# Kernel tuning notes

Measured on AMD Instinct MI355X. Metric: run time of the kernel, lower is better.

Reference implementation:

```python
import jax, jax.numpy as jnp
import numpy as np

N_NODES = 16384
N_EDGES = 65536
N_GRAPHS = 512
F_XD = 78
HEADS = 10
HID = F_XD * HEADS  # 780
SEQ = 1000
EMB = 100
VOCAB = 8000
NF = 32
KS = 8
CLEN = EMB - KS + 1  # 93
OUT_DIM = 128


def setup_inputs():
    key = jax.random.key(0)
    keys = jax.random.split(key, 32)
    it = iter(keys)

    def rn(shape, scale=0.05):
        return jax.random.normal(next(it), shape, dtype=jnp.float32) * scale

    x = jax.random.normal(next(it), (N_NODES, F_XD), dtype=jnp.float32)
    edge_index = jax.random.randint(next(it), (2, N_EDGES), 0, N_NODES)
    batch = jnp.sort(jax.random.randint(next(it), (N_NODES,), 0, N_GRAPHS))
    target = jax.random.randint(next(it), (N_GRAPHS, SEQ), 0, VOCAB)
    return {
        "x": x, "edge_index": edge_index, "batch": batch, "target": target,
        "gat_w": rn((F_XD, HID)), "gat_att_src": rn((HEADS, F_XD)),
        "gat_att_dst": rn((HEADS, F_XD)), "gat_b": rn((HID,)),
        "gcn_w": rn((HID, HID)), "gcn_b": rn((HID,)),
        "fcg1_w": rn((2 * HID, 1500)), "fcg1_b": rn((1500,)),
        "fcg2_w": rn((1500, OUT_DIM)), "fcg2_b": rn((OUT_DIM,)),
        "emb_w": rn((VOCAB, EMB), 1.0),
        "conv_w": rn((NF, SEQ, KS)), "conv_b": rn((NF,)),
        "fcxt_w": rn((NF * CLEN, OUT_DIM)), "fcxt_b": rn((OUT_DIM,)),
        "mlp1_w": rn((2 * OUT_DIM, 1024)), "mlp1_b": rn((1024,)),
        "mlp2_w": rn((1024, 512)), "mlp2_b": rn((512,)),
        "mlp3_w": rn((512, 1)), "mlp3_b": rn((1,)),
    }


def _forward(edge_index, batch, target, x, gat_w, gat_att_src, gat_att_dst, gat_b,
             gcn_w, gcn_b, fcg1_w, fcg1_b, fcg2_w, fcg2_b, emb_w, conv_w, conv_b,
             fcxt_w, fcxt_b, mlp1_w, mlp1_b, mlp2_w, mlp2_b, mlp3_w, mlp3_b):
    loops = jnp.arange(N_NODES)
    src = jnp.concatenate([edge_index[0], loops])  # add self-loops (PyG default)
    dst = jnp.concatenate([edge_index[1], loops])
    # --- GATConv(78 -> 78, heads=10, concat) ---
    xh = (x @ gat_w).reshape(N_NODES, HEADS, F_XD)
    a_src = jnp.einsum('nhc,hc->nh', xh, gat_att_src)
    a_dst = jnp.einsum('nhc,hc->nh', xh, gat_att_dst)
    e = jax.nn.leaky_relu(a_src[src] + a_dst[dst], 0.2)  # [E+N, H]
    emax = jax.ops.segment_max(e, dst, num_segments=N_NODES)
    ee = jnp.exp(e - emax[dst])
    den = jax.ops.segment_sum(ee, dst, num_segments=N_NODES)
    coef = ee / den[dst]  # segment softmax over incoming edges
    h = jax.ops.segment_sum(xh[src] * coef[:, :, None], dst, num_segments=N_NODES)
    h = jax.nn.relu(h.reshape(N_NODES, HID) + gat_b)
    # --- GCNConv(780 -> 780), symmetric normalization with self-loops ---
    hw = h @ gcn_w
    deg = jax.ops.segment_sum(jnp.ones((src.shape[0],), hw.dtype), dst, num_segments=N_NODES)
    dinv = jax.lax.rsqrt(jnp.maximum(deg, 1.0))  # deg >= 1 due to self-loops
    g = jax.ops.segment_sum(hw[src] * (dinv[src] * dinv[dst])[:, None], dst,
                            num_segments=N_NODES) + gcn_b
    g = jax.nn.relu(g)
    # --- global max / mean pool per graph ---
    gmp = jax.ops.segment_max(g, batch, num_segments=N_GRAPHS)
    cnt = jax.ops.segment_sum(jnp.ones((N_NODES,), g.dtype), batch, num_segments=N_GRAPHS)
    gap = jax.ops.segment_sum(g, batch, num_segments=N_GRAPHS) / jnp.maximum(cnt, 1.0)[:, None]
    d = jnp.concatenate([gmp, gap], axis=1)  # [B, 1560]
    d = jax.nn.relu(d @ fcg1_w + fcg1_b)     # dropout = eval-mode no-op
    d = d @ fcg2_w + fcg2_b                  # [B, 128]
    # --- protein branch: embedding + Conv1d(in=1000, out=32, k=8) + fc ---
    emb = emb_w[target]  # [B, SEQ=1000, EMB=100]
    c = jax.lax.conv_general_dilated(emb, conv_w, (1,), 'VALID',
                                     dimension_numbers=('NCH', 'OIH', 'NCH'))
    c = c + conv_b[None, :, None]            # [B, 32, 93]
    p = c.reshape(N_GRAPHS, NF * CLEN) @ fcxt_w + fcxt_b  # [B, 128]
    # --- fused MLP head: 256 -> 1024 -> 512 -> 1 ---
    o = jnp.concatenate([d, p], axis=1)
    o = jax.nn.relu(o @ mlp1_w + mlp1_b)
    o = jax.nn.relu(o @ mlp2_w + mlp2_b)
    return o @ mlp3_w + mlp3_b               # [B, 1]


def reference(x, edge_index, batch, target, gat_w, gat_att_src, gat_att_dst, gat_b,
              gcn_w, gcn_b, fcg1_w, fcg1_b, fcg2_w, fcg2_b, emb_w, conv_w, conv_b,
              fcxt_w, fcxt_b, mlp1_w, mlp1_b, mlp2_w, mlp2_b, mlp3_w, mlp3_b):
    return _forward(edge_index, batch, target, x, gat_w, gat_att_src, gat_att_dst,
                    gat_b, gcn_w, gcn_b, fcg1_w, fcg1_b, fcg2_w, fcg2_b, emb_w,
                    conv_w, conv_b, fcxt_w, fcxt_b, mlp1_w, mlp1_b, mlp2_w, mlp2_b,
                    mlp3_w, mlp3_b)
```

## Files before the change

### kernel.cpp

```cpp
#include <hip/hip_runtime.h>

#define NN 16384
#define NE 65536
#define NT 81920
#define NG 512
#define NH 10
#define FX 78
#define HD 780
#define SEQ 1000
#define EMB 100
#define NF 32
#define KS 8
#define CLEN 93

typedef __bf16 bf16x8 __attribute__((ext_vector_type(8)));
typedef float  f32x4  __attribute__((ext_vector_type(4)));

__device__ inline void load_lds16(const void* g, void* l)
{
    __builtin_amdgcn_global_load_lds(
        (const __attribute__((address_space(1))) void*)g,
        (__attribute__((address_space(3))) void*)l, 16, 0, 0);
}

__device__ inline void bt_one(const float* __restrict__ B, __bf16* __restrict__ out,
                              long idx, int K, int N, int Kp)
{
    int n = idx / Kp, k = idx - (long)(idx / Kp)*Kp;
    out[idx] = (n < N && k < K) ? (__bf16)B[(size_t)k*N + n] : (__bf16)0.f;
}

__global__ __launch_bounds__(256)
void preproc_all(const float* __restrict__ emb_w, __bf16* __restrict__ embbf,
                 const float* __restrict__ conv_w, __bf16* __restrict__ w2,
                 const float* __restrict__ fcg1_w, __bf16* __restrict__ wg1,
                 const float* __restrict__ fcg2_w, __bf16* __restrict__ wg2,
                 const float* __restrict__ fcxt_w, __bf16* __restrict__ wxt,
                 const float* __restrict__ mlp1_w, __bf16* __restrict__ wm1,
                 const float* __restrict__ mlp2_w, __bf16* __restrict__ wm2,
                 const float* __restrict__ x, __bf16* __restrict__ Abf,
                 const float* __restrict__ gat_w, __bf16* __restrict__ wgat,
                 const float* __restrict__ gcn_w, __bf16* __restrict__ wgcn,
                 const int* __restrict__ batch, int* __restrict__ goffs)
{
    long idx = (long)blockIdx.x*256 + threadIdx.x;
    if (idx < 896112L) {
        int r = idx / 112, c = idx - (long)(idx/112)*112;
        embbf[idx] = (__bf16)((r < 8000 && c < EMB) ? emb_w[(size_t)r*EMB + c] : 0.f);
        return;
    }
    idx -= 896112L;
    if (idx < 262144L) {
        int op = idx >> 10, i = idx & 1023;
        int o = op & 31, k = op >> 5;
        w2[idx] = (i < SEQ) ? (__bf16)conv_w[((size_t)o*SEQ + i)*KS + k] : (__bf16)0.f;
        return;
    }
    idx -= 262144L;
    if (idx < 2408448L) { bt_one(fcg1_w, wg1, idx, 1560, 1500, 1568); return; }
    idx -= 2408448L;
    if (idx < 192512L)  { bt_one(fcg2_w, wg2, idx, 1500, 128, 1504); return; }
    idx -= 192512L;
    if (idx < 380928L)  { bt_one(fcxt_w, wxt, idx, 2976, 128, 2976); return; }
    idx -= 380928L;
    if (idx < 262144L)  { bt_one(mlp1_w, wm1, idx, 256, 1024, 256); return; }
    idx -= 262144L;
    if (idx < 524288L)  { bt_one(mlp2_w, wm2, idx, 1024, 512, 1024); return; }
    idx -= 524288L;
    if (idx < 1572864L) {
        int r = idx / 96, c = idx - (long)(idx/96)*96;
        Abf[idx] = (c < FX) ? (__bf16)x[(size_t)r*FX + c] : (__bf16)0.f;
        return;
    }
    idx -= 1572864L;
    if (idx < 86016L)   { bt_one(gat_w, wgat, idx, 78, 780, 96); return; }
    idx -= 86016L;
    if (idx < 716800L)  { bt_one(gcn_w, wgcn, idx, 780, 780, 800); return; }
    idx -= 716800L;
    if (idx <= NG) {
        int b = (int)idx;
        if (b == NG) { goffs[NG] = NN; return; }
        int lo = 0, hi = NN;
        while (lo < hi) { int mid = (lo+hi) >> 1; if (batch[mid] < b) lo = mid+1; else hi = mid; }
        goffs[b] = lo;
    }
}
#define PRE_TOTAL 7302256L
#define PRE_BLOCKS ((PRE_TOTAL + 513 + 255) / 256)

template<bool BIAS, bool RELU, bool BF16OUT>
__global__ __launch_bounds__(512)
void gemm_mfma(const __bf16* __restrict__ A, const __bf16* __restrict__ Bt,
               const float* __restrict__ bias, void* __restrict__ Cv,
               int M, int N, int Kp, int ldc, int Nz)
{
    __shared__ __align__(16) __bf16 As[128*32];
    __shared__ __align__(16) __bf16 Bs[128*32];
    const int tid = threadIdx.x;
    const int nbx = gridDim.x;
    const int lin = blockIdx.y * nbx + blockIdx.x;
    const int per = (nbx * gridDim.y) >> 3;
    const int logical = (lin & 7) * per + (lin >> 3);
    const int row0 = (logical / nbx) * 128, col0 = (logical % nbx) * 128;
    const int lane = tid & 63, wid = tid >> 6;
    const int wm = wid & 3, wn = wid >> 2;
    const int l15 = lane & 15, lk = lane >> 4;
    const int sr  = tid >> 2;
    const int sc8 = (tid & 3) * 8;

    f32x4 acc[2][4];
#pragma unroll
    for (int i = 0; i < 2; i++)
#pragma unroll
        for (int j = 0; j < 4; j++) acc[i][j] = (f32x4){0.f,0.f,0.f,0.f};

    for (int k0 = 0; k0 < Kp; k0 += 32) {
        __syncthreads();
        load_lds16(A  + (size_t)(row0+sr)*Kp + k0 + sc8, &As[wid*512]);
        load_lds16(Bt + (size_t)(col0+sr)*Kp + k0 + sc8, &Bs[wid*512]);
        __syncthreads();
        bf16x8 af[2], bfr[4];
#pragma unroll
        for (int i = 0; i < 2; i++)
            af[i]  = *(const bf16x8*)&As[(wm*32 + i*16 + l15)*32 + lk*8];
#pragma unroll
        for (int j = 0; j < 4; j++)
            bfr[j] = *(const bf16x8*)&Bs[(wn*64 + j*16 + l15)*32 + lk*8];
#pragma unroll
        for (int i = 0; i < 2; i++)
#pragma unroll
            for (int j = 0; j < 4; j++)
                acc[i][j] = __builtin_amdgcn_mfma_f32_16x16x32_bf16(af[i], bfr[j], acc[i][j], 0, 0, 0);
    }

#pragma unroll
    for (int i = 0; i < 2; i++) {
        int rbase = row0 + wm*32 + i*16 + lk*4;
#pragma unroll
        for (int j = 0; j < 4; j++) {
            int cc = col0 + wn*64 + j*16 + l15;
            if (cc >= Nz) continue;
            bool real = cc < N;
            float bv = (BIAS && real) ? bias[cc] : 0.f;
#pragma unroll
            for (int r = 0; r < 4; r++) {
                float v = real ? (acc[i][j][r] + bv) : 0.f;
                if (RELU) v = v > 0.f ? v : 0.f;
                if (BF16OUT) ((__bf16*)Cv)[(size_t)(rbase + r)*ldc + cc] = (__bf16)v;
                else         ((float*) Cv)[(size_t)(rbase + r)*ldc + cc] = v;
            }
        }
    }
}

#define BKP 40
__global__ __launch_bounds__(256)
void gemm_mfma_splitk(const __bf16* __restrict__ A, const __bf16* __restrict__ Bt,
                      float* __restrict__ part, int M, int Kp, int ldp, int ksteps)
{
    __shared__ __align__(16) __bf16 As[128*BKP];
    __shared__ __align__(16) __bf16 Bs[128*BKP];
    const int tid = threadIdx.x;
    const int row0 = blockIdx.y*128, col0 = blockIdx.x*128;
    const int s = blockIdx.z;
    const int lane = tid & 63, wid = tid >> 6;
    const int wm = wid & 1, wn = wid >> 1;
    const int l15 = lane & 15, lk = lane >> 4;

    const int T = Kp >> 5;
    int kb = s*ksteps, ke = kb + ksteps;
    if (ke > T) ke = T;

    f32x4 acc[4][4];
#pragma unroll
    for (int i = 0; i < 4; i++)
#pragma unroll
        for (int j = 0; j < 4; j++) acc[i][j] = (f32x4){0.f,0.f,0.f,0.f};

    for (int kk = kb; kk < ke; kk++) {
        int k0 = kk*32;
        __syncthreads();
#pragma unroll
        for (int it = 0; it < 2; ++it) {
            int c = tid + it*256;
            int r = c >> 2, c16 = c & 3;
            uint4 va = *(const uint4*)(A  + (size_t)(row0+r)*Kp + k0 + c16*8);
            *(uint4*)&As[r*BKP + c16*8] = va;
            uint4 vb = *(const uint4*)(Bt + (size_t)(col0+r)*Kp + k0 + c16*8);
            *(uint4*)&Bs[r*BKP + c16*8] = vb;
        }
        __syncthreads();
        bf16x8 af[4], bfr[4];
#pragma unroll
        for (int i = 0; i < 4; i++) {
            af[i]  = *(const bf16x8*)&As[(wm*64 + i*16 + l15)*BKP + lk*8];
            bfr[i] = *(const bf16x8*)&Bs[(wn*64 + i*16 + l15)*BKP + lk*8];
        }
#pragma unroll
        for (int i = 0; i < 4; i++)
#pragma unroll
            for (int j = 0; j < 4; j++)
                acc[i][j] = __builtin_amdgcn_mfma_f32_16x16x32_bf16(af[i], bfr[j], acc[i][j], 0, 0, 0);
    }

#pragma unroll
    for (int i = 0; i < 4; i++) {
        int rbase = row0 + wm*64 + i*16 + lk*4;
#pragma unroll
        for (int j = 0; j < 4; j++) {
            int cc = col0 + wn*64 + j*16 + l15;
#pragma unroll
            for (int r = 0; r < 4; r++)
                part[((size_t)s*M + rbase + r)*ldp + cc] = acc[i][j][r];
        }
    }
}

template<bool RELU>
__global__ __launch_bounds__(256)
void reduce_splitk(const float* __restrict__ part, const float* __restrict__ bias,
                   __bf16* __restrict__ C, int M, int N, int ldp, int S,
                   int ldc, int Nz)
{
    int idx = blockIdx.x*256 + threadIdx.x;
    int nc4 = Nz >> 2;
    if (idx >= M*nc4) return;
    int r = idx / nc4, c = (idx - r*nc4)*4;
    float4 a = {0.f,0.f,0.f,0.f};
    for (int s = 0; s < S; s++) {
        float4 v = *(const float4*)(part + ((size_t)s*M + r)*ldp + c);
        a.x += v.x; a.y += v.y; a.z += v.z; a.w += v.w;
    }
    float vv[4] = {a.x, a.y, a.z, a.w};
    __bf16 o4[4];
#pragma unroll
    for (int j = 0; j < 4; j++) {
        float v = 0.f;
        if (c + j < N) {
            v = vv[j] + bias[c+j];
            if (RELU) v = v > 0.f ? v : 0.f;
        }
        o4[j] = (__bf16)v;
    }
    *(uint2*)&C[(size_t)r*ldc + c] = *(uint2*)o4;
}

__global__ __launch_bounds__(256)
void attn_logits(const __bf16* __restrict__ xh, const float* __restrict__ att_s,
                 const float* __restrict__ att_d,
                 float* __restrict__ a_src, float* __restrict__ a_dst)
{
    int idx = blockIdx.x*256 + threadIdx.x;
    if (idx >= NN*NH) return;
    int n = idx / NH, h = idx % NH;
    const __bf16* xr = xh + (size_t)n*800 + h*FX;
    const float* as = att_s + h*FX;
    const float* ad = att_d + h*FX;
    float s1 = 0.f, s2 = 0.f;
    for (int c = 0; c < FX; c++) {
        float v = (float)xr[c];
        s1 = fmaf(v, as[c], s1);
        s2 = fmaf(v, ad[c], s2);
    }
    a_src[idx] = s1;
    a_dst[idx] = s2;
}

__global__ void edge_count(const int* __restrict__ ei, int* __restrict__ deg)
{
    int e = blockIdx.x*256 + threadIdx.x;
    if (e >= NT) return;
    int dst = (e < NE) ? ei[NE + e] : (e - NE);
    atomicAdd(&deg[dst], 1);
}

__global__ __launch_bounds__(1024)
void scan_kernel(const int* __restrict__ deg, int* __restrict__ offs,
                 int* __restrict__ cursor, float* __restrict__ dinv)
{
    __shared__ int part[1024];
    int tid = threadIdx.x;
    int base = tid*16;
    int v[16]; int ssum = 0;
#pragma unroll
    for (int j = 0; j < 16; j++) {
        v[j] = deg[base+j];
        dinv[base+j] = rsqrtf((float)(v[j] > 0 ? v[j] : 1));
        ssum += v[j];
    }
    part[tid] = ssum;
    __syncthreads();
    for (int d = 1; d < 1024; d <<= 1) {
        int t = (tid >= d) ? part[tid-d] : 0;
        __syncthreads();
        part[tid] += t;
        __syncthreads();
    }
    int run = (tid == 0) ? 0 : part[tid-1];
#pragma unroll
    for (int j = 0; j < 16; j++) { offs[base+j] = run; cursor[base+j] = run; run += v[j]; }
    if (tid == 1023) offs[NN] = run;
}

__global__ void edge_scatter(const int* __restrict__ ei, int* __restrict__ cursor,
                             int* __restrict__ csr)
{
    int e = blockIdx.x*256 + threadIdx.x;
    if (e >= NT) return;
    int src, dst;
    if (e < NE) { src = ei[e]; dst = ei[NE + e]; }
    else        { src = e - NE; dst = e - NE; }
    int pos = atomicAdd(&cursor[dst], 1);
    csr[pos] = src;
}

__global__ __launch_bounds__(256)
void gat_agg(const __bf16* __restrict__ xh, const float* __restrict__ a_src,
             const float* __restrict__ a_dst, const float* __restrict__ gat_b,
             const int* __restrict__ offs, const int* __restrict__ csr,
             __bf16* __restrict__ hbf)
{
    int n = blockIdx.x*4 + (threadIdx.x >> 6);
    if (n >= NN) return;
    int lane = threadIdx.x & 63;
    bool act = lane < 60;
    int h   = act ? (lane / 6) : 0;
    int sub = act ? (lane % 6) : 0;
    int cbase = h*FX + sub*13;
    int off = offs[n], end = offs[n+1];
    float adn = a_dst[n*NH + h];

    float m = -3.0e38f;
    for (int i = off; i < end; i++) {
        int s = csr[i];
        float ev = a_src[s*NH + h] + adn;
        ev = ev > 0.f ? ev : 0.2f*ev;
        m = fmaxf(m, ev);
    }
    float den = 0.f;
    float acc[13];
#pragma unroll
    for (int j = 0; j < 13; j++) acc[j] = 0.f;
    for (int i = off; i < end; i++) {
        int s = csr[i];
        float ev = a_src[s*NH + h] + adn;
        ev = ev > 0.f ? ev : 0.2f*ev;
        float ee = __expf(ev - m);
        den += ee;
        const __bf16* xr = xh + (size_t)s*800 + cbase;
#pragma unroll
        for (int j = 0; j < 13; j++) acc[j] = fmaf((float)xr[j], ee, acc[j]);
    }
    if (act) {
        float inv = 1.f / den;
        const float* bb = gat_b + cbase;
        __bf16* op = hbf + (size_t)n*800 + cbase;
#pragma unroll
        for (int j = 0; j < 13; j++) {
            float v = fmaf(acc[j], inv, bb[j]);
            op[j] = (__bf16)(v > 0.f ? v : 0.f);
        }
    } else {
        __bf16* op = hbf + (size_t)n*800 + 780 + (lane - 60)*5;
#pragma unroll
        for (int j = 0; j < 5; j++) op[j] = (__bf16)0.f;
    }
}

__global__ __launch_bounds__(256)
void gcn_agg(const __bf16* __restrict__ hw, const float* __restrict__ dinv,
             const float* __restrict__ gcn_b, const int* __restrict__ offs,
             const int* __restrict__ csr, __bf16* __restrict__ g)
{
    int n = blockIdx.x*4 + (threadIdx.x >> 6);
    if (n >= NN) return;
    int lane = threadIdx.x & 63;
    int off = offs[n], end = offs[n+1];
    float dn = dinv[n];
    float acc[13];
#pragma unroll
    for (int j = 0; j < 13; j++) acc[j] = 0.f;
    for (int i = off; i < end; i++) {
        int s = csr[i];
        float w = dinv[s] * dn;
        const __bf16* r = hw + (size_t)s*800;
#pragma unroll
        for (int j = 0; j < 13; j++) {
            int c = lane + 64*j;
            if (c < HD) acc[j] = fmaf((float)r[c], w, acc[j]);
        }
    }
    __bf16* op = g + (size_t)n*HD;
#pragma unroll
    for (int j = 0; j < 13; j++) {
        int c = lane + 64*j;
        if (c < HD) {
            float v = acc[j] + gcn_b[c];
            op[c] = (__bf16)(v > 0.f ? v : 0.f);
        }
    }
}

__global__ __launch_bounds__(256)
void pool_kernel(const __bf16* __restrict__ g, const int* __restrict__ goffs,
                 __bf16* __restrict__ d)
{
    int b = blockIdx.x;
    int tid = threadIdx.x;
    int s = goffs[b], e = goffs[b+1];
    float mx[4], sm[4];
#pragma unroll
    for (int j = 0; j < 4; j++) { mx[j] = -3.0e38f; sm[j] = 0.f; }
    for (int n = s; n < e; n++) {
        const __bf16* r = g + (size_t)n*HD;
#pragma unroll
        for (int j = 0; j < 4; j++) {
            int c = tid + 256*j;
            if (c < HD) { float v = (float)r[c]; mx[j] = fmaxf(mx[j], v); sm[j] += v; }
        }
    }
    int cnt = e - s;
    float inv = 1.f / (float)(cnt > 0 ? cnt : 1);
#pragma unroll
    for (int j = 0; j < 4; j++) {
        int c = tid + 256*j;
        if (c < HD) {
            d[(size_t)b*1568 + c]      = (__bf16)mx[j];
            d[(size_t)b*1568 + HD + c] = (__bf16)(sm[j] * inv);
        }
    }
    if (tid < 8) d[(size_t)b*1568 + 1560 + tid] = (__bf16)0.f;
}

#define CP 104
#define SB (112*40)

__global__ __launch_bounds__(512)
void conv_gemm2(const int* __restrict__ target, const __bf16* __restrict__ embbf,
                const __bf16* __restrict__ w2, const float* __restrict__ conv_b,
                __bf16* __restrict__ cbuf)
{
    __shared__ __align__(16) __bf16 Pl[256*CP];
    __bf16* Bs = Pl;
    int* tg = (int*)&Pl[2*SB];
    const int b = blockIdx.x;
    const int tid = threadIdx.x;
    const int w = tid >> 6, lane = tid & 63;
    const int l15 = lane & 15, lk = lane >> 4;

    for (int i = tid; i < 1024; i += 512)
        tg[i] = ((i < SEQ) ? target[b*SEQ + i] : 8000) * 112;
    __syncthreads();

    const bool st = tid < 448;
    const int sr  = tid & 31;
    const int sch = tid >> 5;

    uint4 sv;
    auto stage_load = [&](int p) {
        if (!st) return;
        sv = *(const uint4*)((const ushort*)embbf + tg[p*32 + sr] + sch*8);
    };
    auto stage_write = [&](int buf) {
        if (!st) return;
        const __bf16* s8 = (const __bf16*)&sv;
        __bf16* base = &Bs[buf*SB + (sch*8)*40 + sr];
#pragma unroll
        for (int j = 0; j < 8; j++) base[j*40] = s8[j];
    };

    f32x4 acc[7][2];
#pragma unroll
    for (int i = 0; i < 7; i++) {
        acc[i][0] = (f32x4){0.f,0.f,0.f,0.f};
        acc[i][1] = (f32x4){0.f,0.f,0.f,0.f};
    }

    const __bf16* w2w0 = w2 + (size_t)(w*32 + l15)*1024 + lk*8;
    const __bf16* w2w1 = w2w0 + (size_t)16*1024;

    stage_load(0);
    stage_write(0);
    int cur = 0;
    for (int p = 0; p < 32; ++p) {
        __syncthreads();
        if (p+1 < 32) stage_load(p+1);
        bf16x8 bf0 = *(const bf16x8*)(w2w0 + p*32);
        bf16x8 bf1 = *(const bf16x8*)(w2w1 + p*32);
        const __bf16* bsc = Bs + cur*SB + lk*8;
        __builtin_amdgcn_s_setprio(1);
#pragma unroll
        for (int mt = 0; mt < 7; mt++) {
            bf16x8 af = *(const bf16x8*)(bsc + (mt*16 + l15)*40);
            acc[mt][0] = __builtin_amdgcn_mfma_f32_16x16x32_bf16(af, bf0, acc[mt][0], 0, 0, 0);
            acc[mt][1] = __builtin_amdgcn_mfma_f32_16x16x32_bf16(af, bf1, acc[mt][1], 0, 0, 0);
        }
        __builtin_amdgcn_s_setprio(0);
        if (p+1 < 32) stage_write(cur^1);
        cur ^= 1;
    }

    __syncthreads();
#pragma unroll
    for (int mt = 0; mt < 7; mt++) {
#pragma unroll
        for (int nt = 0; nt < 2; nt++) {
            int op = w*32 + nt*16 + l15;
            int c0 = mt*16 + lk*4;
            if (c0 >= 100) continue;
            __bf16 o4[4];
#pragma unroll
            for (int rr = 0; rr < 4; rr++) o4[rr] = (__bf16)acc[mt][nt][rr];
            *(uint2*)&Pl[op*CP + c0] = *(uint2*)o4;
        }
    }
    __syncthreads();

    {
        int o = tid & 31, tg16 = tid >> 5;
        float cb = conv_b[o];
#pragma unroll
        for (int j = 0; j < 6; j++) {
            int t = tg16*6 + j;
            if (t >= CLEN) continue;
            float s = cb;
#pragma unroll
            for (int k = 0; k < 8; k++)
                s += (float)Pl[(k*32 + o)*CP + t + k];
            cbuf[(size_t)b*2976 + o*CLEN + t] = (__bf16)s;
        }
    }
}

__global__ __launch_bounds__(256)
void mlp3_dot(const __bf16* __restrict__ o2, const float* __restrict__ w,
              const float* __restrict__ bias, float* __restrict__ out)
{
    int row = blockIdx.x*4 + (threadIdx.x >> 6);
    int lane = threadIdx.x & 63;
    bf16x8 v = *(const bf16x8*)(o2 + (size_t)row*512 + lane*8);
    float4 w0 = *(const float4*)(w + lane*8);
    float4 w1 = *(const float4*)(w + lane*8 + 4);
    float s = (float)v[0]*w0.x + (float)v[1]*w0.y + (float)v[2]*w0.z + (float)v[3]*w0.w
            + (float)v[4]*w1.x + (float)v[5]*w1.y + (float)v[6]*w1.z + (float)v[7]*w1.w;
#pragma unroll
    for (int off = 32; off > 0; off >>= 1) s += __shfl_down(s, off);
    if (lane == 0) out[row] = s + bias[0];
}

extern "C" void kernel_launch(void* const* d_in, const int* in_sizes, int n_in,
                              void* d_out, int out_size, void* d_ws, size_t ws_size,
                              hipStream_t stream)
{
    const float* x      = (const float*)d_in[0];
    const int*   ei     = (const int*)  d_in[1];
    const int*   batch  = (const int*)  d_in[2];
    const int*   target = (const int*)  d_in[3];
    const float* gat_w  = (const float*)d_in[4];
    const float* att_s  = (const float*)d_in[5];
    const float* att_d  = (const float*)d_in[6];
    const float* gat_b  = (const float*)d_in[7];
    const float* gcn_w  = (const float*)d_in[8];
    const float* gcn_b  = (const float*)d_in[9];
    const float* fcg1_w = (const float*)d_in[10];
    const float* fcg1_b = (const float*)d_in[11];
    const float* fcg2_w = (const float*)d_in[12];
    const float* fcg2_b = (const float*)d_in[13];
    const float* emb_w  = (const float*)d_in[14];
    const float* conv_w = (const float*)d_in[15];
    const float* conv_b = (const float*)d_in[16];
    const float* fcxt_w = (const float*)d_in[17];
    const float* fcxt_b = (const float*)d_in[18];
    const float* mlp1_w = (const float*)d_in[19];
    const float* mlp1_b = (const float*)d_in[20];
    const float* mlp2_w = (const float*)d_in[21];
    const float* mlp2_b = (const float*)d_in[22];
    const float* mlp3_w = (const float*)d_in[23];
    const float* mlp3_b = (const float*)d_in[24];
    float* out = (float*)d_out;

    char* ws = (char*)d_ws;
    size_t off = 0;
    auto alloc = [&](size_t bytes) -> char* {
        char* p = ws + off;
        off = (off + bytes + 255) & ~(size_t)255;
        return p;
    };
    __bf16* xhbf  = (__bf16*)alloc((size_t)NN*800*2);
    __bf16* g     = (__bf16*)alloc((size_t)NN*HD*2);
    char*  hbf_rg = alloc((size_t)NN*800*2);
    __bf16* Abf   = (__bf16*)hbf_rg;
    __bf16* hbf   = (__bf16*)hbf_rg;
    float* partial= (float*)hbf_rg;
    __bf16* wgat  = (__bf16*)alloc((size_t)896*96*2);
    __bf16* wgcn  = (__bf16*)alloc((size_t)896*800*2);
    __bf16* wg1   = (__bf16*)alloc((size_t)1536*1568*2);
    __bf16* wg2   = (__bf16*)alloc((size_t)128*1504*2);
    __bf16* wxt   = (__bf16*)alloc((size_t)128*2976*2);
    __bf16* wm1   = (__bf16*)alloc((size_t)1024*256*2);
    __bf16* wm2   = (__bf16*)alloc((size_t)512*1024*2);
    __bf16* convw2= (__bf16*)alloc((size_t)256*1024*2);
    __bf16* embbf = (__bf16*)alloc((size_t)8001*112*2);
    float* a_src  = (float*)alloc((size_t)NN*NH*4);
    float* a_dst  = (float*)alloc((size_t)NN*NH*4);
    int*   deg    = (int*)alloc((size_t)NN*4);
    int*   offs   = (int*)alloc((size_t)(NN+1)*4);
    int*   cursor = (int*)alloc((size_t)NN*4);
    int*   csr    = (int*)alloc((size_t)NT*4);
    float* dinv   = (float*)alloc((size_t)NN*4);
    int*   goffs  = (int*)alloc((size_t)(NG+1)*4);
    __bf16* dpool = (__bf16*)alloc((size_t)NG*1568*2);
    __bf16* d1bf  = (__bf16*)alloc((size_t)NG*1504*2);
    __bf16* cbuf  = (__bf16*)alloc((size_t)NG*NF*CLEN*2);
    __bf16* obuf  = (__bf16*)alloc((size_t)NG*256*2);
    __bf16* o1bf  = (__bf16*)alloc((size_t)NG*1024*2);
    __bf16* o2bf  = (__bf16*)alloc((size_t)NG*512*2);

    __bf16* hwbf = xhbf;

    hipMemsetAsync(deg, 0, (size_t)NN*4, stream);

    preproc_all<<<dim3((unsigned)PRE_BLOCKS), 256, 0, stream>>>(
        emb_w, embbf, conv_w, convw2, fcg1_w, wg1, fcg2_w, wg2, fcxt_w, wxt,
        mlp1_w, wm1, mlp2_w, wm2, x, Abf, gat_w, wgat, gcn_w, wgcn, batch, goffs);

    conv_gemm2<<<dim3(NG), 512, 0, stream>>>(target, embbf, convw2, conv_b, cbuf);

    gemm_mfma<false,false,true>
        <<<dim3(7, NN/128), 512, 0, stream>>>(Abf, wgat, nullptr, xhbf, NN, HD, 96, 800, 800);
    attn_logits<<<dim3((NN*NH+255)/256), 256, 0, stream>>>(xhbf, att_s, att_d, a_src, a_dst);

    edge_count  <<<dim3(NT/256), 256, 0, stream>>>(ei, deg);
    scan_kernel <<<1, 1024, 0, stream>>>(deg, offs, cursor, dinv);
    edge_scatter<<<dim3(NT/256), 256, 0, stream>>>(ei, cursor, csr);

    gat_agg<<<dim3(NN/4), 256, 0, stream>>>(xhbf, a_src, a_dst, gat_b, offs, csr, hbf);

    gemm_mfma<false,false,true>
        <<<dim3(7, NN/128), 512, 0, stream>>>(hbf, wgcn, nullptr, hwbf, NN, HD, 800, 800, 800);
    gcn_agg<<<dim3(NN/4), 256, 0, stream>>>(hwbf, dinv, gcn_b, offs, csr, g);

    pool_kernel<<<NG, 256, 0, stream>>>(g, goffs, dpool);

    gemm_mfma_splitk<<<dim3(12, 4, 4), 256, 0, stream>>>(dpool, wg1, partial, NG, 1568, 1536, 13);
    reduce_splitk<true><<<dim3((NG*(1504/4)+255)/256), 256, 0, stream>>>(partial, fcg1_b, d1bf, NG, 1500, 1536, 4, 1504, 1504);
    gemm_mfma_splitk<<<dim3(1, 4, 12), 256, 0, stream>>>(d1bf, wg2, partial, NG, 1504, 128, 4);
    reduce_splitk<false><<<dim3((NG*32+255)/256), 256, 0, stream>>>(partial, fcg2_b, obuf, NG, 128, 128, 12, 256, 128);
    gemm_mfma_splitk<<<dim3(1, 4, 24), 256, 0, stream>>>(cbuf, wxt, partial, NG, 2976, 128, 4);
    reduce_splitk<false><<<dim3((NG*32+255)/256), 256, 0, stream>>>(partial, fcxt_b, obuf + 128, NG, 128, 128, 24, 256, 128);
    gemm_mfma_splitk<<<dim3(8, 4, 2), 256, 0, stream>>>(obuf, wm1, partial, NG, 256, 1024, 4);
    reduce_splitk<true><<<dim3((NG*256+255)/256), 256, 0, stream>>>(partial, mlp1_b, o1bf, NG, 1024, 1024, 2, 1024, 1024);
    gemm_mfma_splitk<<<dim3(4, 4, 8), 256, 0, stream>>>(o1bf, wm2, partial, NG, 1024, 512, 4);
    reduce_splitk<true><<<dim3((NG*128+255)/256), 256, 0, stream>>>(partial, mlp2_b, o2bf, NG, 512, 512, 8, 512, 512);

    mlp3_dot<<<dim3(NG/4), 256, 0, stream>>>(o2bf, mlp3_w, mlp3_b, out);
}
```

Baseline: 367.4 us.

## Use tiled LDS transpose for weight conversion and double conv K-step

Weight transposes to bf16 move out of the flat per-element preprocessing kernel into a dedicated kernel that stages 32x32 tiles in shared memory. Both the reads and the writes are now coalesced, replacing the strided reads the old version made. Separately, the conv GEMM now stages 64 sequence positions per pipeline step instead of 32, with two 16-byte gathers per thread and a wider LDS stride. This halves the number of barrier-separated iterations at the cost of more LDS and registers, and adds one extra kernel launch.

```diff
diff --git a/kernel.cpp b/kernel.cpp
--- a/kernel.cpp
+++ b/kernel.cpp
@@ -23,24 +23,10 @@
         (__attribute__((address_space(3))) void*)l, 16, 0, 0);
 }
 
-__device__ inline void bt_one(const float* __restrict__ B, __bf16* __restrict__ out,
-                              long idx, int K, int N, int Kp)
-{
-    int n = idx / Kp, k = idx - (long)(idx / Kp)*Kp;
-    out[idx] = (n < N && k < K) ? (__bf16)B[(size_t)k*N + n] : (__bf16)0.f;
-}
-
 __global__ __launch_bounds__(256)
 void preproc_all(const float* __restrict__ emb_w, __bf16* __restrict__ embbf,
                  const float* __restrict__ conv_w, __bf16* __restrict__ w2,
-                 const float* __restrict__ fcg1_w, __bf16* __restrict__ wg1,
-                 const float* __restrict__ fcg2_w, __bf16* __restrict__ wg2,
-                 const float* __restrict__ fcxt_w, __bf16* __restrict__ wxt,
-                 const float* __restrict__ mlp1_w, __bf16* __restrict__ wm1,
-                 const float* __restrict__ mlp2_w, __bf16* __restrict__ wm2,
                  const float* __restrict__ x, __bf16* __restrict__ Abf,
-                 const float* __restrict__ gat_w, __bf16* __restrict__ wgat,
-                 const float* __restrict__ gcn_w, __bf16* __restrict__ wgcn,
                  const int* __restrict__ batch, int* __restrict__ goffs)
 {
     long idx = (long)blockIdx.x*256 + threadIdx.x;
@@ -57,26 +43,12 @@
         return;
     }
     idx -= 262144L;
-    if (idx < 2408448L) { bt_one(fcg1_w, wg1, idx, 1560, 1500, 1568); return; }
-    idx -= 2408448L;
-    if (idx < 192512L)  { bt_one(fcg2_w, wg2, idx, 1500, 128, 1504); return; }
-    idx -= 192512L;
-    if (idx < 380928L)  { bt_one(fcxt_w, wxt, idx, 2976, 128, 2976); return; }
-    idx -= 380928L;
-    if (idx < 262144L)  { bt_one(mlp1_w, wm1, idx, 256, 1024, 256); return; }
-    idx -= 262144L;
-    if (idx < 524288L)  { bt_one(mlp2_w, wm2, idx, 1024, 512, 1024); return; }
-    idx -= 524288L;
     if (idx < 1572864L) {
         int r = idx / 96, c = idx - (long)(idx/96)*96;
         Abf[idx] = (c < FX) ? (__bf16)x[(size_t)r*FX + c] : (__bf16)0.f;
         return;
     }
     idx -= 1572864L;
-    if (idx < 86016L)   { bt_one(gat_w, wgat, idx, 78, 780, 96); return; }
-    idx -= 86016L;
-    if (idx < 716800L)  { bt_one(gcn_w, wgcn, idx, 780, 780, 800); return; }
-    idx -= 716800L;
     if (idx <= NG) {
         int b = (int)idx;
         if (b == NG) { goffs[NG] = NN; return; }
@@ -85,8 +57,44 @@
         goffs[b] = lo;
     }
 }
-#define PRE_TOTAL 7302256L
-#define PRE_BLOCKS ((PRE_TOTAL + 513 + 255) / 256)
+#define PRE_TOTAL 2731633L
+#define PRE_BLOCKS ((PRE_TOTAL + 255) / 256)
+
+__global__ __launch_bounds__(256)
+void transpose_w(const float* __restrict__ fcg1_w, __bf16* __restrict__ wg1,
+                 const float* __restrict__ gcn_w,  __bf16* __restrict__ wgcn,
+                 const float* __restrict__ gat_w,  __bf16* __restrict__ wgat,
+                 const float* __restrict__ fcg2_w, __bf16* __restrict__ wg2,
+                 const float* __restrict__ fcxt_w, __bf16* __restrict__ wxt,
+                 const float* __restrict__ mlp1_w, __bf16* __restrict__ wm1,
+                 const float* __restrict__ mlp2_w, __bf16* __restrict__ wm2)
+{
+    __shared__ float tile[32][33];
+    int t = blockIdx.x;
+    const float* B; __bf16* out; int K, N, Kp, tk_n;
+    if (t < 2352)              { B=fcg1_w; out=wg1;  K=1560; N=1500; Kp=1568; tk_n=49; }
+    else if ((t -= 2352) < 700){ B=gcn_w;  out=wgcn; K=780;  N=780;  Kp=800;  tk_n=25; }
+    else if ((t -= 700) < 84)  { B=gat_w;  out=wgat; K=78;   N=780;  Kp=96;   tk_n=3;  }
+    else if ((t -= 84) < 188)  { B=fcg2_w; out=wg2;  K=1500; N=128;  Kp=1504; tk_n=47; }
+    else if ((t -= 188) < 372) { B=fcxt_w; out=wxt;  K=2976; N=128;  Kp=2976; tk_n=93; }
+    else if ((t -= 372) < 256) { B=mlp1_w; out=wm1;  K=256;  N=1024; Kp=256;  tk_n=8;  }
+    else { t -= 256;             B=mlp2_w; out=wm2;  K=1024; N=512;  Kp=1024; tk_n=32; }
+    int k0 = (t % tk_n) * 32, n0 = (t / tk_n) * 32;
+    int jj = threadIdx.x & 31, ii0 = threadIdx.x >> 5;
+#pragma unroll
+    for (int g = 0; g < 4; g++) {
+        int i = ii0 + g*8;
+        int gk = k0 + i, gn = n0 + jj;
+        tile[i][jj] = (gk < K && gn < N) ? B[(size_t)gk*N + gn] : 0.f;
+    }
+    __syncthreads();
+#pragma unroll
+    for (int g = 0; g < 4; g++) {
+        int i = ii0 + g*8;
+        out[(size_t)(n0 + i)*Kp + k0 + jj] = (__bf16)tile[jj][i];
+    }
+}
+#define TRANS_BLOCKS 4464
 
 template<bool BIAS, bool RELU, bool BF16OUT>
 __global__ __launch_bounds__(512)
@@ -433,7 +441,8 @@
 }
 
 #define CP 104
-#define SB (112*40)
+#define SSTR 76
+#define SB2 (112*SSTR)
 
 __global__ __launch_bounds__(512)
 void conv_gemm2(const int* __restrict__ target, const __bf16* __restrict__ embbf,
@@ -442,7 +451,7 @@
 {
     __shared__ __align__(16) __bf16 Pl[256*CP];
     __bf16* Bs = Pl;
-    int* tg = (int*)&Pl[2*SB];
+    int* tg = (int*)&Pl[2*SB2];
     const int b = blockIdx.x;
     const int tid = threadIdx.x;
     const int w = tid >> 6, lane = tid & 63;
@@ -453,20 +462,25 @@
     __syncthreads();
 
     const bool st = tid < 448;
-    const int sr  = tid & 31;
-    const int sch = tid >> 5;
-
-    uint4 sv;
+    const int r = tid & 63;
+    const int c = (tid >> 6) & 7;
+
+    uint4 sv0, sv1;
     auto stage_load = [&](int p) {
         if (!st) return;
-        sv = *(const uint4*)((const ushort*)embbf + tg[p*32 + sr] + sch*8);
+        const ushort* eb = (const ushort*)embbf + tg[p*64 + r] + c*16;
+        sv0 = *(const uint4*)(eb);
+        sv1 = *(const uint4*)(eb + 8);
     };
     auto stage_write = [&](int buf) {
         if (!st) return;
-        const __bf16* s8 = (const __bf16*)&sv;
-        __bf16* base = &Bs[buf*SB + (sch*8)*40 + sr];
-#pragma unroll
-        for (int j = 0; j < 8; j++) base[j*40] = s8[j];
+        const __bf16* s8a = (const __bf16*)&sv0;
+        const __bf16* s8b = (const __bf16*)&sv1;
+        __bf16* base = &Bs[buf*SB2 + (c*16)*SSTR + r];
+#pragma unroll
+        for (int j = 0; j < 8; j++) base[j*SSTR] = s8a[j];
+#pragma unroll
+        for (int j = 0; j < 8; j++) base[(8+j)*SSTR] = s8b[j];
     };
 
     f32x4 acc[7][2];
@@ -482,21 +496,24 @@
     stage_load(0);
     stage_write(0);
     int cur = 0;
-    for (int p = 0; p < 32; ++p) {
+    for (int p = 0; p < 16; ++p) {
         __syncthreads();
-        if (p+1 < 32) stage_load(p+1);
-        bf16x8 bf0 = *(const bf16x8*)(w2w0 + p*32);
-        bf16x8 bf1 = *(const bf16x8*)(w2w1 + p*32);
-        const __bf16* bsc = Bs + cur*SB + lk*8;
+        if (p+1 < 16) stage_load(p+1);
+        const __bf16* bsc = Bs + cur*SB2 + lk*8;
         __builtin_amdgcn_s_setprio(1);
 #pragma unroll
-        for (int mt = 0; mt < 7; mt++) {
-            bf16x8 af = *(const bf16x8*)(bsc + (mt*16 + l15)*40);
-            acc[mt][0] = __builtin_amdgcn_mfma_f32_16x16x32_bf16(af, bf0, acc[mt][0], 0, 0, 0);
-            acc[mt][1] = __builtin_amdgcn_mfma_f32_16x16x32_bf16(af, bf1, acc[mt][1], 0, 0, 0);
+        for (int k32 = 0; k32 < 2; k32++) {
+            bf16x8 bf0 = *(const bf16x8*)(w2w0 + p*64 + k32*32);
+            bf16x8 bf1 = *(const bf16x8*)(w2w1 + p*64 + k32*32);
+#pragma unroll
+            for (int mt = 0; mt < 7; mt++) {
+                bf16x8 af = *(const bf16x8*)(bsc + (mt*16 + l15)*SSTR + k32*32);
+                acc[mt][0] = __builtin_amdgcn_mfma_f32_16x16x32_bf16(af, bf0, acc[mt][0], 0, 0, 0);
+                acc[mt][1] = __builtin_amdgcn_mfma_f32_16x16x32_bf16(af, bf1, acc[mt][1], 0, 0, 0);
+            }
         }
         __builtin_amdgcn_s_setprio(0);
-        if (p+1 < 32) stage_write(cur^1);
+        if (p+1 < 16) stage_write(cur^1);
         cur ^= 1;
     }
 
@@ -621,8 +638,10 @@
     hipMemsetAsync(deg, 0, (size_t)NN*4, stream);
 
     preproc_all<<<dim3((unsigned)PRE_BLOCKS), 256, 0, stream>>>(
-        emb_w, embbf, conv_w, convw2, fcg1_w, wg1, fcg2_w, wg2, fcxt_w, wxt,
-        mlp1_w, wm1, mlp2_w, wm2, x, Abf, gat_w, wgat, gcn_w, wgcn, batch, goffs);
+        emb_w, embbf, conv_w, convw2, x, Abf, batch, goffs);
+    transpose_w<<<dim3(TRANS_BLOCKS), 256, 0, stream>>>(
+        fcg1_w, wg1, gcn_w, wgcn, gat_w, wgat, fcg2_w, wg2,
+        fcxt_w, wxt, mlp1_w, wm1, mlp2_w, wm2);
 
     conv_gemm2<<<dim3(NG), 512, 0, stream>>>(target, embbf, convw2, conv_b, cbuf);
 
```

Result: slower. 416.2 us (+13.3%).
